# Optimization experiments

Measured on AMD Instinct MI355X. Metric: run time of the kernel, lower is better.

## Reference

```python
import jax, jax.numpy as jnp
import numpy as np

CS = [32, 32, 64, 128, 256, 256, 128, 96, 96]
NC = 19
N0, N1, N2, N3, N4 = 50000, 20000, 8000, 3200, 1300


def build_shapes():
    cs = CS
    def rb(ci, co):
        t = [(27, ci, co), (27, co, co)]
        if ci != co:
            t.append((ci, co))  # 1x1 shortcut conv
        return t
    s = [(27, 4, cs[0]), (27, cs[0], cs[0])]                       # stem
    s += [(8, cs[0], cs[0])] + rb(cs[0], cs[1]) + rb(cs[1], cs[1])  # stage1
    s += [(8, cs[1], cs[1])] + rb(cs[1], cs[2]) + rb(cs[2], cs[2])  # stage2
    s += [(8, cs[2], cs[2])] + rb(cs[2], cs[3]) + rb(cs[3], cs[3])  # stage3
    s += [(8, cs[3], cs[3])] + rb(cs[3], cs[4]) + rb(cs[4], cs[4])  # stage4
    s += [(8, cs[4], cs[5])] + rb(cs[5] + cs[3], cs[5]) + rb(cs[5], cs[5])  # up1
    s += [(8, cs[5], cs[6])] + rb(cs[6] + cs[2], cs[6]) + rb(cs[6], cs[6])  # up2
    s += [(8, cs[6], cs[7])] + rb(cs[7] + cs[1], cs[7]) + rb(cs[7], cs[7])  # up3
    s += [(8, cs[7], cs[8])] + rb(cs[8] + cs[0], cs[8]) + rb(cs[8], cs[8])  # up4
    s += [(cs[8], NC), (NC,), (cs[8], cs[8]), (cs[8],), (cs[8], 128), (128,)]
    return s

P_TOTAL = sum(int(np.prod(sh)) for sh in build_shapes())


def _bn(x):
    # train-mode BatchNorm, gamma=1 beta=0 (set by weight_initialization)
    return (x - x.mean(0)) * jax.lax.rsqrt(jnp.var(x, 0) + 1e-5)


def _spconv(x, nbr, W):
    # sparse conv as gather-GEMM-scatter over K kernel offsets.
    # x: [Nin, Cin], nbr: [Nout, K] row indices into x, W: [K, Cin, Cout]
    acc0 = jnp.zeros((nbr.shape[0], W.shape[-1]), x.dtype)
    def step(acc, kw):
        idx, Wk = kw
        return acc + x[idx] @ Wk, None
    acc, _ = jax.lax.scan(step, acc0, (nbr.T, W))
    return acc


def _spdeconv(x, parent, off, W):
    # transposed ks=2 stride=2 conv: each fine voxel has exactly one coarse
    # parent and one kernel-offset id. out[i] = x[parent[i]] @ W[off[i]]
    y = jnp.einsum('nc,kcd->nkd', x[parent], W)  # [Nf, 8, Cout]
    return jnp.take_along_axis(y, off[:, None, None], axis=1)[:, 0, :]


def _cbr(x, nbr, W):
    return jax.nn.relu(_bn(_spconv(x, nbr, W)))


def _resblock(x, nbr, take, ci, co):
    w1 = take(); w2 = take()
    h = _bn(_spconv(jax.nn.relu(_bn(_spconv(x, nbr, w1))), nbr, w2))
    s = x if ci == co else _bn(x @ take())
    return jax.nn.relu(h + s)


def _forward(x, nbr0, nbr1, nbr2, nbr3, nbr4, d1, d2, d3, d4,
             u1p, u1o, u2p, u2o, u3p, u3o, u4p, u4o, params):
    parts = []
    o = 0
    for sh in build_shapes():
        n = int(np.prod(sh))
        parts.append(params[o:o + n].reshape(sh))
        o += n
    it = iter(parts)
    take = lambda: next(it)
    cs = CS
    x0 = _cbr(x, nbr0, take()); x0 = _cbr(x0, nbr0, take())            # stem
    h = _cbr(x0, d1, take())
    h = _resblock(h, nbr1, take, cs[0], cs[1]); x1 = _resblock(h, nbr1, take, cs[1], cs[1])
    h = _cbr(x1, d2, take())
    h = _resblock(h, nbr2, take, cs[1], cs[2]); x2 = _resblock(h, nbr2, take, cs[2], cs[2])
    h = _cbr(x2, d3, take())
    h = _resblock(h, nbr3, take, cs[2], cs[3]); x3 = _resblock(h, nbr3, take, cs[3], cs[3])
    h = _cbr(x3, d4, take())
    h = _resblock(h, nbr4, take, cs[3], cs[4]); x4 = _resblock(h, nbr4, take, cs[4], cs[4])
    y = jax.nn.relu(_bn(_spdeconv(x4, u1p, u1o, take())))
    y = jnp.concatenate([y, x3], 1)
    y = _resblock(y, nbr3, take, cs[5] + cs[3], cs[5]); y = _resblock(y, nbr3, take, cs[5], cs[5])
    y = jax.nn.relu(_bn(_spdeconv(y, u2p, u2o, take())))
    y = jnp.concatenate([y, x2], 1)
    y = _resblock(y, nbr2, take, cs[6] + cs[2], cs[6]); y = _resblock(y, nbr2, take, cs[6], cs[6])
    y = jax.nn.relu(_bn(_spdeconv(y, u3p, u3o, take())))
    y = jnp.concatenate([y, x1], 1)
    y = _resblock(y, nbr1, take, cs[7] + cs[1], cs[7]); y = _resblock(y, nbr1, take, cs[7], cs[7])
    y = jax.nn.relu(_bn(_spdeconv(y, u4p, u4o, take())))
    y = jnp.concatenate([y, x0], 1)
    y = _resblock(y, nbr0, take, cs[8] + cs[0], cs[8]); y = _resblock(y, nbr0, take, cs[8], cs[8])
    wc = take(); bc = take(); w1 = take(); b1 = take(); w2 = take(); b2 = take()
    out = y @ wc + bc                             # classifier logits [N0, NC]
    feat = jax.nn.relu(y @ w1 + b1) @ w2 + b2     # projection head [N0, 128]
    return out, feat


def setup_inputs() -> dict:
    key = jax.random.key(0)
    ks = jax.random.split(key, 20)
    ri = lambda k, shape, hi: jax.random.randint(k, shape, 0, hi, dtype=jnp.int32)
    return {
        'x': jax.random.normal(ks[0], (N0, 4), jnp.float32),
        'nbr0': ri(ks[1], (N0, 27), N0), 'nbr1': ri(ks[2], (N1, 27), N1),
        'nbr2': ri(ks[3], (N2, 27), N2), 'nbr3': ri(ks[4], (N3, 27), N3),
        'nbr4': ri(ks[5], (N4, 27), N4),
        'd1': ri(ks[6], (N1, 8), N0), 'd2': ri(ks[7], (N2, 8), N1),
        'd3': ri(ks[8], (N3, 8), N2), 'd4': ri(ks[9], (N4, 8), N3),
        'u1p': ri(ks[10], (N3,), N4), 'u1o': ri(ks[11], (N3,), 8),
        'u2p': ri(ks[12], (N2,), N3), 'u2o': ri(ks[13], (N2,), 8),
        'u3p': ri(ks[14], (N1,), N2), 'u3o': ri(ks[15], (N1,), 8),
        'u4p': ri(ks[16], (N0,), N1), 'u4o': ri(ks[17], (N0,), 8),
        'params': jax.random.normal(ks[18], (P_TOTAL,), jnp.float32) * 0.05,
    }


def reference(x, nbr0, nbr1, nbr2, nbr3, nbr4, d1, d2, d3, d4,
              u1p, u1o, u2p, u2o, u3p, u3o, u4p, u4o, params):
    return _forward(x, nbr0, nbr1, nbr2, nbr3, nbr4, d1, d2, d3, d4,
                    u1p, u1o, u2p, u2o, u3p, u3o, u4p, u4o, params)
```

## Files before the change

kernel.cpp:

```cpp
#include <hip/hip_runtime.h>
#include <hip/hip_bf16.h>
#include <stdint.h>

typedef __hip_bfloat16 hbf;
typedef unsigned short u16;
typedef __attribute__((ext_vector_type(8))) short bfrag;
typedef __attribute__((ext_vector_type(4))) float f4;

#define NP0 50000
#define NP1 20000
#define NP2 8000
#define NP3 3200
#define NP4 1300

static inline int cdiv(int a, int b) { return (a + b - 1) / b; }

static __device__ __forceinline__ float u2f(u16 u) { return __uint_as_float(((unsigned)u) << 16); }
static __device__ __forceinline__ u16 f2u(float f) {
  hbf h = __float2bfloat16(f);
  u16 r; __builtin_memcpy(&r, &h, 2); return r;
}
static __device__ __forceinline__ float pload(const void* P, int isbf, size_t i) {
  return isbf ? u2f(((const u16*)P)[i]) : ((const float*)P)[i];
}

__global__ void k_sniff(const void* __restrict__ xraw, int* __restrict__ flagp) {
  __shared__ float smax[256];
  const u16* u = (const u16*)xraw;
  float m = 0.f;
  for (int i = threadIdx.x; i < 2048; i += 256) {
    float v = u2f(u[2 * i]);
    if (isnan(v) || isinf(v)) m = 1e30f; else m = fmaxf(m, fabsf(v));
  }
  smax[threadIdx.x] = m;
  __syncthreads();
  for (int s = 128; s > 0; s >>= 1) {
    if (threadIdx.x < s) smax[threadIdx.x] = fmaxf(smax[threadIdx.x], smax[threadIdx.x + s]);
    __syncthreads();
  }
  if (threadIdx.x == 0) *flagp = (smax[0] < 1e4f) ? 1 : 0;
}

__global__ __launch_bounds__(256) void k_prep_frag(
    const void* __restrict__ P, const int* __restrict__ flagp, u16* __restrict__ W,
    long src, long halfel, int K, int CI, int CO, int CB32, int NT16)
{
  int f = *flagp;
  long total = (long)K * CB32 * NT16 * 64;
  for (long c = (long)blockIdx.x * 256 + threadIdx.x; c < total; c += (long)gridDim.x * 256) {
    int lane = (int)(c & 63); long t = c >> 6;
    int nt = (int)(t % NT16); t /= NT16;
    int cb = (int)(t % CB32); int k = (int)(t / CB32);
    int co = nt * 16 + (lane & 15);
    int cib = cb * 32 + (lane >> 4) * 8;
    u16 hi[8], lo[8];
#pragma unroll
    for (int j = 0; j < 8; ++j) {
      int ci = cib + j; float v = 0.f;
      if (ci < CI && co < CO) v = pload(P, f, src + ((size_t)k * CI + ci) * CO + co);
      u16 h = f2u(v);
      hi[j] = h;
      lo[j] = f2u(v - u2f(h));
    }
    *(bfrag*)(W + c * 8) = *(const bfrag*)hi;
    *(bfrag*)(W + halfel + c * 8) = *(const bfrag*)lo;
  }
}

__global__ void k_prep_bias(const void* __restrict__ P, const int* __restrict__ flagp,
                            float* __restrict__ B, long src, int n)
{
  int f = *flagp;
  int i = blockIdx.x * 256 + threadIdx.x;
  if (i < n) B[i] = pload(P, f, src + i);
}

__global__ void k_pad(const void* __restrict__ xraw, const int* __restrict__ flagp,
                      float* __restrict__ Xp, int N)
{
  int f = *flagp; int total = N * 32;
  for (int i = blockIdx.x * 256 + threadIdx.x; i < total; i += gridDim.x * 256) {
    int n = i >> 5, cc = i & 31;
    Xp[i] = (cc < 4) ? pload(xraw, f, (size_t)n * 4 + cc) : 0.f;
  }
}

template<int NT>
__global__ __launch_bounds__(256) void k_conv_mfma(
    const float* __restrict__ X, const int* __restrict__ nbr,
    const u16* __restrict__ Wp, long halfel, float* __restrict__ Y,
    const float* __restrict__ bias, int relu,
    int N, int K, int CB32, int NT16, int CO, int XS, int tlen, int atomic)
{
  const int lane = threadIdx.x & 63;
  const int wv = threadIdx.x >> 6;
  const int rowbase = blockIdx.x * 128 + wv * 32;
  const int ntb = blockIdx.y * NT;
  const int ml = lane & 15;
  const int quad = lane >> 4;
  const int ktot = K * CB32;
  const int t0 = blockIdx.z * tlen;
  const int t1 = (t0 + tlen < ktot) ? (t0 + tlen) : ktot;

  f4 acc[2][NT];
#pragma unroll
  for (int i = 0; i < 2; ++i)
#pragma unroll
    for (int j = 0; j < NT; ++j) acc[i][j] = (f4)(0.f);

  int k = t0 / CB32;
  int cb = t0 - k * CB32;
  int idx[2];
  bool fresh = true;

  for (int t = t0; t < t1; ++t) {
    if (fresh) {
#pragma unroll
      for (int mt = 0; mt < 2; ++mt) {
        int r = rowbase + mt * 16 + ml;
        idx[mt] = (r < N) ? (nbr ? nbr[(size_t)r * K + k] : r) : 0;
      }
      fresh = false;
    }
    const u16* WH = Wp + (size_t)t * NT16 * 512;
    const u16* WL = WH + halfel;
    bfrag bh[NT], bl[NT];
#pragma unroll
    for (int nt = 0; nt < NT; ++nt) {
      size_t o = ((size_t)(ntb + nt) * 64 + lane) * 8;
      bh[nt] = *(const bfrag*)(WH + o);
      bl[nt] = *(const bfrag*)(WL + o);
    }
    bfrag ahi[2], alo[2];
#pragma unroll
    for (int mt = 0; mt < 2; ++mt) {
      const float* ap = X + (size_t)idx[mt] * XS + cb * 32 + quad * 8;
      float4 q0 = *(const float4*)ap;
      float4 q1 = *(const float4*)(ap + 4);
      float av[8] = {q0.x, q0.y, q0.z, q0.w, q1.x, q1.y, q1.z, q1.w};
      u16 hi8[8], lo8[8];
#pragma unroll
      for (int j = 0; j < 8; ++j) {
        u16 hh = f2u(av[j]);
        hi8[j] = hh;
        lo8[j] = f2u(av[j] - u2f(hh));
      }
      __builtin_memcpy(&ahi[mt], hi8, 16);
      __builtin_memcpy(&alo[mt], lo8, 16);
    }
#pragma unroll
    for (int mt = 0; mt < 2; ++mt)
#pragma unroll
      for (int nt = 0; nt < NT; ++nt) {
        acc[mt][nt] = __builtin_amdgcn_mfma_f32_16x16x32_bf16(alo[mt], bh[nt], acc[mt][nt], 0, 0, 0);
        acc[mt][nt] = __builtin_amdgcn_mfma_f32_16x16x32_bf16(ahi[mt], bl[nt], acc[mt][nt], 0, 0, 0);
        acc[mt][nt] = __builtin_amdgcn_mfma_f32_16x16x32_bf16(ahi[mt], bh[nt], acc[mt][nt], 0, 0, 0);
      }
    if (++cb == CB32) { cb = 0; ++k; fresh = true; }
  }

#pragma unroll
  for (int mt = 0; mt < 2; ++mt) {
#pragma unroll
    for (int nt = 0; nt < NT; ++nt) {
      int col = (ntb + nt) * 16 + ml;
      if (col >= CO) continue;
      float bvv = bias ? bias[col] : 0.f;
#pragma unroll
      for (int reg = 0; reg < 4; ++reg) {
        int row = rowbase + mt * 16 + quad * 4 + reg;
        if (row < N) {
          if (atomic) {
            atomicAdd(&Y[(size_t)row * CO + col], acc[mt][nt][reg]);
          } else {
            float v = acc[mt][nt][reg] + bvv;
            if (relu) v = fmaxf(v, 0.f);
            Y[(size_t)row * CO + col] = v;
          }
        }
      }
    }
  }
}

__global__ void k_bias_relu(float* __restrict__ Y, const float* __restrict__ bias,
                            int relu, int total, int CO)
{
  int stride = gridDim.x * 256;
  for (int i = blockIdx.x * 256 + threadIdx.x; i < total; i += stride) {
    int c = i % CO;
    float v = Y[i] + (bias ? bias[c] : 0.f);
    if (relu) v = fmaxf(v, 0.f);
    Y[i] = v;
  }
}

static void launch_conv(hipStream_t s, int bx, const float* X, const int* nbr,
                        const u16* W, long halfel, float* Y, const float* bias, int relu,
                        int N, int K, int CB32, int NT16, int CO, int XS)
{
  int NT = (NT16 % 6 == 0) ? 6 : ((NT16 % 4 == 0) ? 4 : 2);
  int ny = NT16 / NT;
  int ktot = K * CB32;
  long blocks = (long)bx * ny;
  int ZS = 1;
  if (ktot > 1) {
    ZS = (int)((1024 + blocks - 1) / blocks);
    if (ZS > ktot) ZS = ktot;
    if (ZS < 1) ZS = 1;
  }
  int tlen = cdiv(ktot, ZS);
  ZS = cdiv(ktot, tlen);
  int atomic = (ZS > 1) ? 1 : 0;
  if (atomic) hipMemsetAsync(Y, 0, (size_t)N * CO * 4, s);
  dim3 g(bx, ny, ZS);
  if (NT == 6)      k_conv_mfma<6><<<g, 256, 0, s>>>(X, nbr, W, halfel, Y, bias, relu, N, K, CB32, NT16, CO, XS, tlen, atomic);
  else if (NT == 4) k_conv_mfma<4><<<g, 256, 0, s>>>(X, nbr, W, halfel, Y, bias, relu, N, K, CB32, NT16, CO, XS, tlen, atomic);
  else              k_conv_mfma<2><<<g, 256, 0, s>>>(X, nbr, W, halfel, Y, bias, relu, N, K, CB32, NT16, CO, XS, tlen, atomic);
  if (atomic && (bias || relu)) {
    int total = N * CO;
    int nb = cdiv(total, 1024); if (nb > 1024) nb = 1024; if (nb < 1) nb = 1;
    k_bias_relu<<<nb, 256, 0, s>>>(Y, bias, relu, total, CO);
  }
}

__global__ __launch_bounds__(256) void k_deconv(
    const float* __restrict__ X, const int* __restrict__ par, const int* __restrict__ off,
    const void* __restrict__ P, long wofs, const int* __restrict__ flagp,
    float* __restrict__ Y, int N, int CI, int CO)
{
  int f = *flagp;
  int lane = threadIdx.x & 63, wv = threadIdx.x >> 6;
  int n = blockIdx.y * 4 + wv; if (n >= N) return;
  int co = blockIdx.x * 64 + lane; if (co >= CO) return;
  const float* xr = X + (size_t)par[n] * CI;
  size_t wbase = wofs + (size_t)off[n] * CI * CO + co;
  float acc = 0.f;
  for (int ci = 0; ci < CI; ci += 4) {
    float4 xv = *(const float4*)(xr + ci);
    acc += xv.x * pload(P, f, wbase + (size_t)ci * CO);
    acc += xv.y * pload(P, f, wbase + (size_t)(ci + 1) * CO);
    acc += xv.z * pload(P, f, wbase + (size_t)(ci + 2) * CO);
    acc += xv.w * pload(P, f, wbase + (size_t)(ci + 3) * CO);
  }
  Y[(size_t)n * CO + co] = acc;
}

__global__ __launch_bounds__(256) void k_bn_stats(
    const float* __restrict__ X, float* __restrict__ st, int total, int C)
{
  __shared__ float ssum[384], ssq[384];
  for (int c = threadIdx.x; c < C; c += 256) { ssum[c] = 0.f; ssq[c] = 0.f; }
  __syncthreads();
  int gid = blockIdx.x * 256 + threadIdx.x;
  int total4 = total >> 2;
  int stride = gridDim.x * 256;
  int c0 = (gid * 4) % C;
  float s0 = 0.f, s1 = 0.f, s2 = 0.f, s3 = 0.f;
  float q0 = 0.f, q1 = 0.f, q2 = 0.f, q3 = 0.f;
  for (int i = gid; i < total4; i += stride) {
    float4 v = ((const float4*)X)[i];
    s0 += v.x; q0 += v.x * v.x;
    s1 += v.y; q1 += v.y * v.y;
    s2 += v.z; q2 += v.z * v.z;
    s3 += v.w; q3 += v.w * v.w;
  }
  atomicAdd(&ssum[c0], s0);     atomicAdd(&ssq[c0], q0);
  atomicAdd(&ssum[c0 + 1], s1); atomicAdd(&ssq[c0 + 1], q1);
  atomicAdd(&ssum[c0 + 2], s2); atomicAdd(&ssq[c0 + 2], q2);
  atomicAdd(&ssum[c0 + 3], s3); atomicAdd(&ssq[c0 + 3], q3);
  __syncthreads();
  for (int c = threadIdx.x; c < C; c += 256) {
    atomicAdd(&st[c], ssum[c]); atomicAdd(&st[384 + c], ssq[c]);
  }
}

__global__ __launch_bounds__(256) void k_bn_apply(
    const float* __restrict__ X, const float* __restrict__ st, const float* __restrict__ add,
    float* __restrict__ Y, int relu, int total, int C, float invN)
{
  __shared__ float mean[384], rsig[384];
  for (int c = threadIdx.x; c < C; c += 256) {
    float mm = st[c] * invN;
    float vv = st[384 + c] * invN - mm * mm;
    mean[c] = mm; rsig[c] = rsqrtf(vv + 1e-5f);
  }
  __syncthreads();
  int gid = blockIdx.x * 256 + threadIdx.x;
  int total4 = total >> 2;
  int stride = gridDim.x * 256;
  int c0 = (gid * 4) % C;
  float m0 = mean[c0], m1 = mean[c0 + 1], m2 = mean[c0 + 2], m3 = mean[c0 + 3];
  float r0 = rsig[c0], r1 = rsig[c0 + 1], r2 = rsig[c0 + 2], r3 = rsig[c0 + 3];
  for (int i = gid; i < total4; i += stride) {
    float4 v = ((const float4*)X)[i];
    v.x = (v.x - m0) * r0; v.y = (v.y - m1) * r1;
    v.z = (v.z - m2) * r2; v.w = (v.w - m3) * r3;
    if (add) {
      float4 a = ((const float4*)add)[i];
      v.x += a.x; v.y += a.y; v.z += a.z; v.w += a.w;
    }
    if (relu) {
      v.x = fmaxf(v.x, 0.f); v.y = fmaxf(v.y, 0.f);
      v.z = fmaxf(v.z, 0.f); v.w = fmaxf(v.w, 0.f);
    }
    ((float4*)Y)[i] = v;
  }
}

__global__ void k_copycols(const float* __restrict__ S, float* __restrict__ D,
                           int N, int Cs, int Cd, int off)
{
  int csq = Cs >> 2;
  int total4 = N * csq;
  int stride = gridDim.x * 256;
  for (int i = blockIdx.x * 256 + threadIdx.x; i < total4; i += stride) {
    int n = i / csq, cc = i - n * csq;
    ((float4*)D)[((size_t)n * Cd + off) / 4 + cc] = ((const float4*)S)[i];
  }
}

__global__ void k_store_dyn(const float* __restrict__ S, void* __restrict__ D,
                            const int* __restrict__ flagp, size_t eofs, int n)
{
  int f = *flagp;
  int n4 = n >> 2;
  int stride = gridDim.x * 256;
  for (int i = blockIdx.x * 256 + threadIdx.x; i < n4; i += stride) {
    float4 v = ((const float4*)S)[i];
    if (f) {
      ushort4 u;
      u.x = f2u(v.x); u.y = f2u(v.y); u.z = f2u(v.z); u.w = f2u(v.w);
      *(ushort4*)((u16*)D + eofs + (size_t)i * 4) = u;
    } else {
      *(float4*)((float*)D + eofs + (size_t)i * 4) = v;
    }
  }
}


extern "C" void kernel_launch(void* const* d_in, const int* in_sizes, int n_in,
                              void* d_out, int out_size, void* d_ws, size_t ws_size,
                              hipStream_t stream)
{
  const void* xraw = d_in[0];
  const int* nbr0 = (const int*)d_in[1];
  const int* nbr1 = (const int*)d_in[2];
  const int* nbr2 = (const int*)d_in[3];
  const int* nbr3 = (const int*)d_in[4];
  const int* nbr4 = (const int*)d_in[5];
  const int* d1 = (const int*)d_in[6];
  const int* d2 = (const int*)d_in[7];
  const int* d3 = (const int*)d_in[8];
  const int* d4 = (const int*)d_in[9];
  const int* u1p = (const int*)d_in[10]; const int* u1o = (const int*)d_in[11];
  const int* u2p = (const int*)d_in[12]; const int* u2o = (const int*)d_in[13];
  const int* u3p = (const int*)d_in[14]; const int* u3o = (const int*)d_in[15];
  const int* u4p = (const int*)d_in[16]; const int* u4o = (const int*)d_in[17];
  const void* params = d_in[18];
  (void)in_sizes; (void)n_in;

  char* base = (char*)d_ws; size_t off = 0;
  auto ab = [&](size_t bytes) -> void* { void* p = base + off; off += (bytes + 63) & ~(size_t)63; return p; };
  int* flagp = (int*)ab(64);
  float* st = (float*)ab((size_t)64 * 768 * 4);
  u16* Wst = (u16*)ab((size_t)5400000 * 2);
  float* Bstf = (float*)ab((size_t)512 * 4);
  float* x0 = (float*)ab((size_t)NP0 * 32 * 4);
  float* x1 = (float*)ab((size_t)NP1 * 32 * 4);
  float* x2 = (float*)ab((size_t)NP2 * 64 * 4);
  float* x3 = (float*)ab((size_t)NP3 * 128 * 4);
  float* x4 = (float*)ab((size_t)NP4 * 256 * 4);
  float* U  = (float*)ab((size_t)NP0 * 96 * 4);
  float* A  = (float*)ab((size_t)NP0 * 96 * 4);
  float* B  = (float*)ab((size_t)NP0 * 128 * 4);
  float* Xp = B;
  if (off > ws_size) { hipMemsetAsync(d_out, 0, (size_t)out_size * 2, stream); return; }

  long po = 0;
  int bnc = 0;

  auto prepF = [&](int K, int CI, int CO, int CB32, int NT16) -> long {
    long chunks = (long)K * CB32 * NT16 * 64;
    long halfel = chunks * 8;
    int nb = (int)((chunks + 255) / 256); if (nb > 4096) nb = 4096; if (nb < 1) nb = 1;
    k_prep_frag<<<nb, 256, 0, stream>>>(params, flagp, Wst, po, halfel, K, CI, CO, CB32, NT16);
    po += (long)K * CI * CO;
    return halfel;
  };
  auto convop = [&](const float* X, const int* nb_, int K, int CI, int CO, float* Y, int N, int XS) {
    int CB32 = cdiv(CI, 32), NT16 = cdiv(CO, 16);
    long halfel = prepF(K, CI, CO, CB32, NT16);
    launch_conv(stream, cdiv(N, 128), X, nb_, Wst, halfel, Y, nullptr, 0, N, K, CB32, NT16, CO, XS);
  };
  auto linop = [&](const float* X, int CI, int CO, float* Y, int N, bool bias, int relu) {
    int CB32 = cdiv(CI, 32), NT16 = cdiv(CO, 16);
    long halfel = prepF(1, CI, CO, CB32, NT16);
    const float* bp = nullptr;
    if (bias) {
      k_prep_bias<<<cdiv(CO, 256), 256, 0, stream>>>(params, flagp, Bstf, po, CO);
      po += CO; bp = Bstf;
    }
    launch_conv(stream, cdiv(N, 128), X, nullptr, Wst, halfel, Y, bp, relu, N, 1, CB32, NT16, CO, CI);
  };
  auto deconvop = [&](const float* X, const int* par, const int* ofv, int CI, int CO, float* Y, int N) {
    long wofs = po; po += (long)8 * CI * CO;
    dim3 g(cdiv(CO, 64), cdiv(N, 4));
    k_deconv<<<g, 256, 0, stream>>>(X, par, ofv, params, wofs, flagp, Y, N, CI, CO);
  };
  auto bnop = [&](const float* X, int N, int C, const float* add, int relu, float* out) {
    float* slot = st + (size_t)(bnc++) * 768;
    int total = N * C;
    int total4 = total >> 2;
    int nb1 = cdiv(total4, 4096); if (nb1 > 504) nb1 = 504; if (nb1 < 3) nb1 = 3;
    nb1 = ((nb1 + 2) / 3) * 3;
    k_bn_stats<<<nb1, 256, 0, stream>>>(X, slot, total, C);
    int nb2 = cdiv(total4, 2048); if (nb2 > 510) nb2 = 510; if (nb2 < 3) nb2 = 3;
    nb2 = ((nb2 + 2) / 3) * 3;
    k_bn_apply<<<nb2, 256, 0, stream>>>(X, slot, add, out ? out : (float*)X, relu, total, C, 1.0f / (float)N);
  };
  auto copyop = [&](const float* S, float* D, int N, int Cs, int Cd, int o2) {
    int total4 = (N * Cs) >> 2;
    int nb3 = cdiv(total4, 1024); if (nb3 > 1024) nb3 = 1024; if (nb3 < 1) nb3 = 1;
    k_copycols<<<nb3, 256, 0, stream>>>(S, D, N, Cs, Cd, o2);
  };
  auto storeop = [&](const float* S, size_t eo, int n) {
    int nb4 = cdiv(n >> 2, 1024); if (nb4 > 1024) nb4 = 1024; if (nb4 < 1) nb4 = 1;
    k_store_dyn<<<nb4, 256, 0, stream>>>(S, d_out, flagp, eo, n);
  };
  auto resblock = [&](const int* nb, int N, int CI, int CO,
                      float* H, float* t1, float* t2, float* OUT) {
    convop(H, nb, 27, CI, CO, t1, N, CI);
    bnop(t1, N, CO, nullptr, 1, nullptr);
    convop(t1, nb, 27, CO, CO, t2, N, CO);
    const float* S;
    if (CI == CO) S = H;
    else { linop(H, CI, CO, t1, N, false, 0); bnop(t1, N, CO, nullptr, 0, nullptr); S = t1; }
    bnop(t2, N, CO, S, 1, OUT);
  };

  k_sniff<<<1, 256, 0, stream>>>(xraw, flagp);
  hipMemsetAsync(st, 0, (size_t)64 * 768 * 4, stream);
  k_pad<<<1024, 256, 0, stream>>>(xraw, flagp, Xp, NP0);

  convop(Xp, nbr0, 27, 4, 32, A, NP0, 32);  bnop(A, NP0, 32, nullptr, 1, nullptr);
  convop(A, nbr0, 27, 32, 32, x0, NP0, 32); bnop(x0, NP0, 32, nullptr, 1, nullptr);
  convop(x0, d1, 8, 32, 32, U, NP1, 32); bnop(U, NP1, 32, nullptr, 1, nullptr);
  resblock(nbr1, NP1, 32, 32, U, A, B, U);
  resblock(nbr1, NP1, 32, 32, U, A, B, x1);
  convop(x1, d2, 8, 32, 32, U, NP2, 32); bnop(U, NP2, 32, nullptr, 1, nullptr);
  resblock(nbr2, NP2, 32, 64, U, A, B, U);
  resblock(nbr2, NP2, 64, 64, U, A, B, x2);
  convop(x2, d3, 8, 64, 64, U, NP3, 64); bnop(U, NP3, 64, nullptr, 1, nullptr);
  resblock(nbr3, NP3, 64, 128, U, A, B, U);
  resblock(nbr3, NP3, 128, 128, U, A, B, x3);
  convop(x3, d4, 8, 128, 128, U, NP4, 128); bnop(U, NP4, 128, nullptr, 1, nullptr);
  resblock(nbr4, NP4, 128, 256, U, A, B, U);
  resblock(nbr4, NP4, 256, 256, U, A, B, x4);
  deconvop(x4, u1p, u1o, 256, 256, A, NP3); bnop(A, NP3, 256, nullptr, 1, nullptr);
  copyop(A, B, NP3, 256, 384, 0); copyop(x3, B, NP3, 128, 384, 256);
  resblock(nbr3, NP3, 384, 256, B, A, U, B);
  resblock(nbr3, NP3, 256, 256, B, A, U, U);
  deconvop(U, u2p, u2o, 256, 128, A, NP2); bnop(A, NP2, 128, nullptr, 1, nullptr);
  copyop(A, B, NP2, 128, 192, 0); copyop(x2, B, NP2, 64, 192, 128);
  resblock(nbr2, NP2, 192, 128, B, A, U, B);
  resblock(nbr2, NP2, 128, 128, B, A, U, U);
  deconvop(U, u3p, u3o, 128, 96, A, NP1); bnop(A, NP1, 96, nullptr, 1, nullptr);
  copyop(A, B, NP1, 96, 128, 0); copyop(x1, B, NP1, 32, 128, 96);
  resblock(nbr1, NP1, 128, 96, B, A, U, B);
  resblock(nbr1, NP1, 96, 96, B, A, U, U);
  deconvop(U, u4p, u4o, 96, 96, A, NP0); bnop(A, NP0, 96, nullptr, 1, nullptr);
  copyop(A, B, NP0, 96, 128, 0); copyop(x0, B, NP0, 32, 128, 96);
  resblock(nbr0, NP0, 128, 96, B, A, U, B);
  resblock(nbr0, NP0, 96, 96, B, A, U, U);
  linop(U, 96, 19, x0, NP0, true, 0);
  linop(U, 96, 96, A, NP0, true, 1);
  linop(A, 96, 128, B, NP0, true, 0);
  storeop(x0, 0, NP0 * 19);
  storeop(B, (size_t)NP0 * 19, NP0 * 128);
}
```

Baseline: 4.423 ms.

## Store activations as pre-split bf16 hi/lo pairs to skip in-conv splitting

New measurement: 4.590 ms. 1.04x slower.

```diff
diff --git a/kernel.cpp b/kernel.cpp
--- a/kernel.cpp
+++ b/kernel.cpp
@@ -23,6 +23,7 @@
 static __device__ __forceinline__ float pload(const void* P, int isbf, size_t i) {
   return isbf ? u2f(((const u16*)P)[i]) : ((const float*)P)[i];
 }
+
 
 __global__ void k_sniff(const void* __restrict__ xraw, int* __restrict__ flagp) {
   __shared__ float smax[256];
@@ -76,18 +77,21 @@
 }
 
 __global__ void k_pad(const void* __restrict__ xraw, const int* __restrict__ flagp,
-                      float* __restrict__ Xp, int N)
+                      u16* __restrict__ Xp2, int N)
 {
   int f = *flagp; int total = N * 32;
   for (int i = blockIdx.x * 256 + threadIdx.x; i < total; i += gridDim.x * 256) {
     int n = i >> 5, cc = i & 31;
-    Xp[i] = (cc < 4) ? pload(xraw, f, (size_t)n * 4 + cc) : 0.f;
+    float v = (cc < 4) ? pload(xraw, f, (size_t)n * 4 + cc) : 0.f;
+    u16 h = f2u(v);
+    Xp2[(size_t)n * 64 + cc] = h;
+    Xp2[(size_t)n * 64 + 32 + cc] = f2u(v - u2f(h));
   }
 }
 
 template<int NT>
 __global__ __launch_bounds__(256) void k_conv_mfma(
-    const float* __restrict__ X, const int* __restrict__ nbr,
+    const u16* __restrict__ X, const int* __restrict__ nbr,
     const u16* __restrict__ Wp, long halfel, float* __restrict__ Y,
     const float* __restrict__ bias, int relu,
     int N, int K, int CB32, int NT16, int CO, int XS, int tlen, int atomic)
@@ -134,19 +138,9 @@
     bfrag ahi[2], alo[2];
 #pragma unroll
     for (int mt = 0; mt < 2; ++mt) {
-      const float* ap = X + (size_t)idx[mt] * XS + cb * 32 + quad * 8;
-      float4 q0 = *(const float4*)ap;
-      float4 q1 = *(const float4*)(ap + 4);
-      float av[8] = {q0.x, q0.y, q0.z, q0.w, q1.x, q1.y, q1.z, q1.w};
-      u16 hi8[8], lo8[8];
-#pragma unroll
-      for (int j = 0; j < 8; ++j) {
-        u16 hh = f2u(av[j]);
-        hi8[j] = hh;
-        lo8[j] = f2u(av[j] - u2f(hh));
-      }
-      __builtin_memcpy(&ahi[mt], hi8, 16);
-      __builtin_memcpy(&alo[mt], lo8, 16);
+      const u16* ap = X + (size_t)idx[mt] * (2 * XS) + cb * 32 + quad * 8;
+      ahi[mt] = *(const bfrag*)ap;
+      alo[mt] = *(const bfrag*)(ap + XS);
     }
 #pragma unroll
     for (int mt = 0; mt < 2; ++mt)
@@ -195,7 +189,34 @@
   }
 }
 
-static void launch_conv(hipStream_t s, int bx, const float* X, const int* nbr,
+__global__ void k_bias_relu_split(const float* __restrict__ Y, const float* __restrict__ bias,
+                                  u16* __restrict__ D2, int relu, int N, int CO)
+{
+  int co4 = CO >> 2;
+  int total4 = N * co4;
+  int stride = gridDim.x * 256;
+  for (int i = blockIdx.x * 256 + threadIdx.x; i < total4; i += stride) {
+    int n = i / co4, c = (i - n * co4) * 4;
+    float4 v = ((const float4*)Y)[i];
+    float vv[4] = {v.x, v.y, v.z, v.w};
+    ushort4 h, l;
+    u16 hh[4], ll[4];
+#pragma unroll
+    for (int j = 0; j < 4; ++j) {
+      float x = vv[j] + (bias ? bias[c + j] : 0.f);
+      if (relu) x = fmaxf(x, 0.f);
+      u16 hu = f2u(x);
+      hh[j] = hu; ll[j] = f2u(x - u2f(hu));
+    }
+    h.x = hh[0]; h.y = hh[1]; h.z = hh[2]; h.w = hh[3];
+    l.x = ll[0]; l.y = ll[1]; l.z = ll[2]; l.w = ll[3];
+    size_t ho = (size_t)n * 2 * CO + c;
+    *(ushort4*)(D2 + ho) = h;
+    *(ushort4*)(D2 + ho + CO) = l;
+  }
+}
+
+static void launch_conv(hipStream_t s, int bx, const u16* X, const int* nbr,
                         const u16* W, long halfel, float* Y, const float* bias, int relu,
                         int N, int K, int CB32, int NT16, int CO, int XS)
 {
@@ -225,7 +246,7 @@
 }
 
 __global__ __launch_bounds__(256) void k_deconv(
-    const float* __restrict__ X, const int* __restrict__ par, const int* __restrict__ off,
+    const u16* __restrict__ X2, const int* __restrict__ par, const int* __restrict__ off,
     const void* __restrict__ P, long wofs, const int* __restrict__ flagp,
     float* __restrict__ Y, int N, int CI, int CO)
 {
@@ -233,15 +254,16 @@
   int lane = threadIdx.x & 63, wv = threadIdx.x >> 6;
   int n = blockIdx.y * 4 + wv; if (n >= N) return;
   int co = blockIdx.x * 64 + lane; if (co >= CO) return;
-  const float* xr = X + (size_t)par[n] * CI;
+  const u16* xr = X2 + (size_t)par[n] * 2 * CI;
   size_t wbase = wofs + (size_t)off[n] * CI * CO + co;
   float acc = 0.f;
   for (int ci = 0; ci < CI; ci += 4) {
-    float4 xv = *(const float4*)(xr + ci);
-    acc += xv.x * pload(P, f, wbase + (size_t)ci * CO);
-    acc += xv.y * pload(P, f, wbase + (size_t)(ci + 1) * CO);
-    acc += xv.z * pload(P, f, wbase + (size_t)(ci + 2) * CO);
-    acc += xv.w * pload(P, f, wbase + (size_t)(ci + 3) * CO);
+    ushort4 xh = *(const ushort4*)(xr + ci);
+    ushort4 xl = *(const ushort4*)(xr + CI + ci);
+    acc += (u2f(xh.x) + u2f(xl.x)) * pload(P, f, wbase + (size_t)ci * CO);
+    acc += (u2f(xh.y) + u2f(xl.y)) * pload(P, f, wbase + (size_t)(ci + 1) * CO);
+    acc += (u2f(xh.z) + u2f(xl.z)) * pload(P, f, wbase + (size_t)(ci + 2) * CO);
+    acc += (u2f(xh.w) + u2f(xl.w)) * pload(P, f, wbase + (size_t)(ci + 3) * CO);
   }
   Y[(size_t)n * CO + co] = acc;
 }
@@ -276,8 +298,8 @@
 }
 
 __global__ __launch_bounds__(256) void k_bn_apply(
-    const float* __restrict__ X, const float* __restrict__ st, const float* __restrict__ add,
-    float* __restrict__ Y, int relu, int total, int C, float invN)
+    const float* __restrict__ X, const float* __restrict__ st, const u16* __restrict__ add2,
+    u16* __restrict__ Y2, int relu, int total, int C, float invN)
 {
   __shared__ float mean[384], rsig[384];
   for (int c = threadIdx.x; c < C; c += 256) {
@@ -289,34 +311,49 @@
   int gid = blockIdx.x * 256 + threadIdx.x;
   int total4 = total >> 2;
   int stride = gridDim.x * 256;
-  int c0 = (gid * 4) % C;
+  int C4 = C >> 2;
+  int c0 = (gid % C4) * 4;
+  int n = gid / C4;
+  int dn = stride / C4;
   float m0 = mean[c0], m1 = mean[c0 + 1], m2 = mean[c0 + 2], m3 = mean[c0 + 3];
   float r0 = rsig[c0], r1 = rsig[c0 + 1], r2 = rsig[c0 + 2], r3 = rsig[c0 + 3];
-  for (int i = gid; i < total4; i += stride) {
+  for (int i = gid; i < total4; i += stride, n += dn) {
     float4 v = ((const float4*)X)[i];
-    v.x = (v.x - m0) * r0; v.y = (v.y - m1) * r1;
-    v.z = (v.z - m2) * r2; v.w = (v.w - m3) * r3;
-    if (add) {
-      float4 a = ((const float4*)add)[i];
-      v.x += a.x; v.y += a.y; v.z += a.z; v.w += a.w;
+    float w0 = (v.x - m0) * r0, w1 = (v.y - m1) * r1;
+    float w2 = (v.z - m2) * r2, w3 = (v.w - m3) * r3;
+    size_t ho = (size_t)n * 2 * C + c0;
+    if (add2) {
+      ushort4 ah = *(const ushort4*)(add2 + ho);
+      ushort4 al = *(const ushort4*)(add2 + ho + C);
+      w0 += u2f(ah.x) + u2f(al.x); w1 += u2f(ah.y) + u2f(al.y);
+      w2 += u2f(ah.z) + u2f(al.z); w3 += u2f(ah.w) + u2f(al.w);
     }
     if (relu) {
-      v.x = fmaxf(v.x, 0.f); v.y = fmaxf(v.y, 0.f);
-      v.z = fmaxf(v.z, 0.f); v.w = fmaxf(v.w, 0.f);
-    }
-    ((float4*)Y)[i] = v;
-  }
-}
-
-__global__ void k_copycols(const float* __restrict__ S, float* __restrict__ D,
+      w0 = fmaxf(w0, 0.f); w1 = fmaxf(w1, 0.f);
+      w2 = fmaxf(w2, 0.f); w3 = fmaxf(w3, 0.f);
+    }
+    u16 h0 = f2u(w0), h1 = f2u(w1), h2 = f2u(w2), h3 = f2u(w3);
+    ushort4 hh; hh.x = h0; hh.y = h1; hh.z = h2; hh.w = h3;
+    ushort4 ll;
+    ll.x = f2u(w0 - u2f(h0)); ll.y = f2u(w1 - u2f(h1));
+    ll.z = f2u(w2 - u2f(h2)); ll.w = f2u(w3 - u2f(h3));
+    *(ushort4*)(Y2 + ho) = hh;
+    *(ushort4*)(Y2 + ho + C) = ll;
+  }
+}
+
+__global__ void k_copycols(const u16* __restrict__ S2, u16* __restrict__ D2,
                            int N, int Cs, int Cd, int off)
 {
   int csq = Cs >> 2;
   int total4 = N * csq;
   int stride = gridDim.x * 256;
   for (int i = blockIdx.x * 256 + threadIdx.x; i < total4; i += stride) {
-    int n = i / csq, cc = i - n * csq;
-    ((float4*)D)[((size_t)n * Cd + off) / 4 + cc] = ((const float4*)S)[i];
+    int n = i / csq, cc = (i - n * csq) * 4;
+    size_t so = (size_t)n * 2 * Cs + cc;
+    size_t dd = (size_t)n * 2 * Cd + off + cc;
+    *(ushort4*)(D2 + dd) = *(const ushort4*)(S2 + so);
+    *(ushort4*)(D2 + dd + Cd) = *(const ushort4*)(S2 + so + Cs);
   }
 }
 
@@ -366,15 +403,15 @@
   float* st = (float*)ab((size_t)64 * 768 * 4);
   u16* Wst = (u16*)ab((size_t)5400000 * 2);
   float* Bstf = (float*)ab((size_t)512 * 4);
-  float* x0 = (float*)ab((size_t)NP0 * 32 * 4);
-  float* x1 = (float*)ab((size_t)NP1 * 32 * 4);
-  float* x2 = (float*)ab((size_t)NP2 * 64 * 4);
-  float* x3 = (float*)ab((size_t)NP3 * 128 * 4);
-  float* x4 = (float*)ab((size_t)NP4 * 256 * 4);
+  u16* x0 = (u16*)ab((size_t)NP0 * 32 * 4);
+  u16* x1 = (u16*)ab((size_t)NP1 * 32 * 4);
+  u16* x2 = (u16*)ab((size_t)NP2 * 64 * 4);
+  u16* x3 = (u16*)ab((size_t)NP3 * 128 * 4);
+  u16* x4 = (u16*)ab((size_t)NP4 * 256 * 4);
   float* U  = (float*)ab((size_t)NP0 * 96 * 4);
   float* A  = (float*)ab((size_t)NP0 * 96 * 4);
   float* B  = (float*)ab((size_t)NP0 * 128 * 4);
-  float* Xp = B;
+  u16* Xp = (u16*)B;
   if (off > ws_size) { hipMemsetAsync(d_out, 0, (size_t)out_size * 2, stream); return; }
 
   long po = 0;
@@ -388,12 +425,12 @@
     po += (long)K * CI * CO;
     return halfel;
   };
-  auto convop = [&](const float* X, const int* nb_, int K, int CI, int CO, float* Y, int N, int XS) {
+  auto convop = [&](const u16* X2, const int* nb_, int K, int CI, int CO, float* Y, int N, int XS) {
     int CB32 = cdiv(CI, 32), NT16 = cdiv(CO, 16);
     long halfel = prepF(K, CI, CO, CB32, NT16);
-    launch_conv(stream, cdiv(N, 128), X, nb_, Wst, halfel, Y, nullptr, 0, N, K, CB32, NT16, CO, XS);
-  };
-  auto linop = [&](const float* X, int CI, int CO, float* Y, int N, bool bias, int relu) {
+    launch_conv(stream, cdiv(N, 128), X2, nb_, Wst, halfel, Y, nullptr, 0, N, K, CB32, NT16, CO, XS);
+  };
+  auto linop = [&](const u16* X2, int CI, int CO, float* Y, int N, bool bias, int relu, u16* osplit) {
     int CB32 = cdiv(CI, 32), NT16 = cdiv(CO, 16);
     long halfel = prepF(1, CI, CO, CB32, NT16);
     const float* bp = nullptr;
@@ -401,14 +438,20 @@
       k_prep_bias<<<cdiv(CO, 256), 256, 0, stream>>>(params, flagp, Bstf, po, CO);
       po += CO; bp = Bstf;
     }
-    launch_conv(stream, cdiv(N, 128), X, nullptr, Wst, halfel, Y, bp, relu, N, 1, CB32, NT16, CO, CI);
-  };
-  auto deconvop = [&](const float* X, const int* par, const int* ofv, int CI, int CO, float* Y, int N) {
+    if (osplit) {
+      launch_conv(stream, cdiv(N, 128), X2, nullptr, Wst, halfel, Y, nullptr, 0, N, 1, CB32, NT16, CO, CI);
+      int nb = cdiv((N * CO) >> 2, 1024); if (nb > 1024) nb = 1024; if (nb < 1) nb = 1;
+      k_bias_relu_split<<<nb, 256, 0, stream>>>(Y, bp, osplit, relu, N, CO);
+    } else {
+      launch_conv(stream, cdiv(N, 128), X2, nullptr, Wst, halfel, Y, bp, relu, N, 1, CB32, NT16, CO, CI);
+    }
+  };
+  auto deconvop = [&](const u16* X2, const int* par, const int* ofv, int CI, int CO, float* Y, int N) {
     long wofs = po; po += (long)8 * CI * CO;
     dim3 g(cdiv(CO, 64), cdiv(N, 4));
-    k_deconv<<<g, 256, 0, stream>>>(X, par, ofv, params, wofs, flagp, Y, N, CI, CO);
-  };
-  auto bnop = [&](const float* X, int N, int C, const float* add, int relu, float* out) {
+    k_deconv<<<g, 256, 0, stream>>>(X2, par, ofv, params, wofs, flagp, Y, N, CI, CO);
+  };
+  auto bnop = [&](const float* X, int N, int C, const u16* add2, int relu, u16* out2) {
     float* slot = st + (size_t)(bnc++) * 768;
     int total = N * C;
     int total4 = total >> 2;
@@ -417,12 +460,12 @@
     k_bn_stats<<<nb1, 256, 0, stream>>>(X, slot, total, C);
     int nb2 = cdiv(total4, 2048); if (nb2 > 510) nb2 = 510; if (nb2 < 3) nb2 = 3;
     nb2 = ((nb2 + 2) / 3) * 3;
-    k_bn_apply<<<nb2, 256, 0, stream>>>(X, slot, add, out ? out : (float*)X, relu, total, C, 1.0f / (float)N);
-  };
-  auto copyop = [&](const float* S, float* D, int N, int Cs, int Cd, int o2) {
+    k_bn_apply<<<nb2, 256, 0, stream>>>(X, slot, add2, out2, relu, total, C, 1.0f / (float)N);
+  };
+  auto copyop = [&](const u16* S2, u16* D2, int N, int Cs, int Cd, int o2) {
     int total4 = (N * Cs) >> 2;
     int nb3 = cdiv(total4, 1024); if (nb3 > 1024) nb3 = 1024; if (nb3 < 1) nb3 = 1;
-    k_copycols<<<nb3, 256, 0, stream>>>(S, D, N, Cs, Cd, o2);
+    k_copycols<<<nb3, 256, 0, stream>>>(S2, D2, N, Cs, Cd, o2);
   };
   auto storeop = [&](const float* S, size_t eo, int n) {
     int nb4 = cdiv(n >> 2, 1024); if (nb4 > 1024) nb4 = 1024; if (nb4 < 1) nb4 = 1;
@@ -430,52 +473,58 @@
   };
   auto resblock = [&](const int* nb, int N, int CI, int CO,
                       float* H, float* t1, float* t2, float* OUT) {
-    convop(H, nb, 27, CI, CO, t1, N, CI);
-    bnop(t1, N, CO, nullptr, 1, nullptr);
-    convop(t1, nb, 27, CO, CO, t2, N, CO);
-    const float* S;
-    if (CI == CO) S = H;
-    else { linop(H, CI, CO, t1, N, false, 0); bnop(t1, N, CO, nullptr, 0, nullptr); S = t1; }
-    bnop(t2, N, CO, S, 1, OUT);
+    convop((const u16*)H, nb, 27, CI, CO, t1, N, CI);
+    bnop(t1, N, CO, nullptr, 1, (u16*)t2);
+    convop((const u16*)t2, nb, 27, CO, CO, t1, N, CO);
+    if (CI == CO) {
+      bnop(t1, N, CO, (const u16*)H, 1, (u16*)OUT);
+    } else {
+      linop((const u16*)H, CI, CO, t2, N, false, 0, nullptr);
+      bnop(t2, N, CO, nullptr, 0, (u16*)OUT);
+      bnop(t1, N, CO, (const u16*)OUT, 1, (u16*)OUT);
+    }
   };
 
   k_sniff<<<1, 256, 0, stream>>>(xraw, flagp);
   hipMemsetAsync(st, 0, (size_t)64 * 768 * 4, stream);
   k_pad<<<1024, 256, 0, stream>>>(xraw, flagp, Xp, NP0);
 
-  convop(Xp, nbr0, 27, 4, 32, A, NP0, 32);  bnop(A, NP0, 32, nullptr, 1, nullptr);
-  convop(A, nbr0, 27, 32, 32, x0, NP0, 32); bnop(x0, NP0, 32, nullptr, 1, nullptr);
-  convop(x0, d1, 8, 32, 32, U, NP1, 32); bnop(U, NP1, 32, nullptr, 1, nullptr);
+  convop(Xp, nbr0, 27, 4, 32, U, NP0, 32);
+  bnop(U, NP0, 32, nullptr, 1, (u16*)A);
+  convop((const u16*)A, nbr0, 27, 32, 32, U, NP0, 32);
+  bnop(U, NP0, 32, nullptr, 1, x0);
+  convop(x0, d1, 8, 32, 32, A, NP1, 32); bnop(A, NP1, 32, nullptr, 1, (u16*)U);
   resblock(nbr1, NP1, 32, 32, U, A, B, U);
-  resblock(nbr1, NP1, 32, 32, U, A, B, x1);
-  convop(x1, d2, 8, 32, 32, U, NP2, 32); bnop(U, NP2, 32, nullptr, 1, nullptr);
+  resblock(nbr1, NP1, 32, 32, U, A, B, (float*)x1);
+  convop(x1, d2, 8, 32, 32, A, NP2, 32); bnop(A, NP2, 32, nullptr, 1, (u16*)U);
   resblock(nbr2, NP2, 32, 64, U, A, B, U);
-  resblock(nbr2, NP2, 64, 64, U, A, B, x2);
-  convop(x2, d3, 8, 64, 64, U, NP3, 64); bnop(U, NP3, 64, nullptr, 1, nullptr);
+  resblock(nbr2, NP2, 64, 64, U, A, B, (float*)x2);
+  convop(x2, d3, 8, 64, 64, A, NP3, 64); bnop(A, NP3, 64, nullptr, 1, (u16*)U);
   resblock(nbr3, NP3, 64, 128, U, A, B, U);
-  resblock(nbr3, NP3, 128, 128, U, A, B, x3);
-  convop(x3, d4, 8, 128, 128, U, NP4, 128); bnop(U, NP4, 128, nullptr, 1, nullptr);
+  resblock(nbr3, NP3, 128, 128, U, A, B, (float*)x3);
+  convop(x3, d4, 8, 128, 128, A, NP4, 128); bnop(A, NP4, 128, nullptr, 1, (u16*)U);
   resblock(nbr4, NP4, 128, 256, U, A, B, U);
-  resblock(nbr4, NP4, 256, 256, U, A, B, x4);
-  deconvop(x4, u1p, u1o, 256, 256, A, NP3); bnop(A, NP3, 256, nullptr, 1, nullptr);
-  copyop(A, B, NP3, 256, 384, 0); copyop(x3, B, NP3, 128, 384, 256);
+  resblock(nbr4, NP4, 256, 256, U, A, B, (float*)x4);
+  deconvop(x4, u1p, u1o, 256, 256, A, NP3); bnop(A, NP3, 256, nullptr, 1, (u16*)U);
+  copyop((u16*)U, (u16*)B, NP3, 256, 384, 0); copyop(x3, (u16*)B, NP3, 128, 384, 256);
   resblock(nbr3, NP3, 384, 256, B, A, U, B);
   resblock(nbr3, NP3, 256, 256, B, A, U, U);
-  deconvop(U, u2p, u2o, 256, 128, A, NP2); bnop(A, NP2, 128, nullptr, 1, nullptr);
-  copyop(A, B, NP2, 128, 192, 0); copyop(x2, B, NP2, 64, 192, 128);
+  deconvop((const u16*)U, u2p, u2o, 256, 128, A, NP2); bnop(A, NP2, 128, nullptr, 1, (u16*)U);
+  copyop((u16*)U, (u16*)B, NP2, 128, 192, 0); copyop(x2, (u16*)B, NP2, 64, 192, 128);
   resblock(nbr2, NP2, 192, 128, B, A, U, B);
   resblock(nbr2, NP2, 128, 128, B, A, U, U);
-  deconvop(U, u3p, u3o, 128, 96, A, NP1); bnop(A, NP1, 96, nullptr, 1, nullptr);
-  copyop(A, B, NP1, 96, 128, 0); copyop(x1, B, NP1, 32, 128, 96);
+  deconvop((const u16*)U, u3p, u3o, 128, 96, A, NP1); bnop(A, NP1, 96, nullptr, 1, (u16*)U);
+  copyop((u16*)U, (u16*)B, NP1, 96, 128, 0); copyop(x1, (u16*)B, NP1, 32, 128, 96);
   resblock(nbr1, NP1, 128, 96, B, A, U, B);
   resblock(nbr1, NP1, 96, 96, B, A, U, U);
-  deconvop(U, u4p, u4o, 96, 96, A, NP0); bnop(A, NP0, 96, nullptr, 1, nullptr);
-  copyop(A, B, NP0, 96, 128, 0); copyop(x0, B, NP0, 32, 128, 96);
+  deconvop((const u16*)U, u4p, u4o, 96, 96, A, NP0); bnop(A, NP0, 96, nullptr, 1, (u16*)U);
+  copyop((u16*)U, (u16*)B, NP0, 96, 128, 0); copyop(x0, (u16*)B, NP0, 32, 128, 96);
   resblock(nbr0, NP0, 128, 96, B, A, U, B);
   resblock(nbr0, NP0, 96, 96, B, A, U, U);
-  linop(U, 96, 19, x0, NP0, true, 0);
-  linop(U, 96, 96, A, NP0, true, 1);
-  linop(A, 96, 128, B, NP0, true, 0);
-  storeop(x0, 0, NP0 * 19);
+  float* x0f = (float*)x0;
+  linop((const u16*)U, 96, 19, x0f, NP0, true, 0, nullptr);
+  linop((const u16*)U, 96, 96, B, NP0, true, 1, (u16*)A);
+  linop((const u16*)A, 96, 128, B, NP0, true, 0, nullptr);
+  storeop(x0f, 0, NP0 * 19);
   storeop(B, (size_t)NP0 * 19, NP0 * 128);
 }
```
